# Optimization experiments

Hardware: AMD Instinct MI355X
Metric: run time of the kernel (lower is better)

## Reference

```python
import jax, jax.numpy as jnp
import numpy as np

DIM_HEAD = 128
HEADS = 16
SCALE = DIM_HEAD ** -0.5


def rotate_half(t):
    # '... (j d) -> ... j d' with j=2: split into first/second halves
    x1, x2 = jnp.split(t, 2, axis=-1)
    return jnp.concatenate((-x2, x1), axis=-1)


def apply_rope(pos, t):
    # pos: [n, d]; t: [..., n, d]
    return t * jnp.cos(pos) + rotate_half(t) * jnp.sin(pos)


def setup_inputs() -> dict:
    key = jax.random.key(0)
    k0, k1, k2, k3 = jax.random.split(key, 4)
    b, n, dim = 2, 2048, 2048
    inner = HEADS * DIM_HEAD
    return {
        "x": jax.random.normal(k0, (b, n, dim), jnp.float32),
        "Wq": jax.random.normal(k1, (dim, inner), jnp.float32) * 0.02,
        "Wkv": jax.random.normal(k2, (dim, 2 * DIM_HEAD), jnp.float32) * 0.02,
        "Wout": jax.random.normal(k3, (inner, dim), jnp.float32) * 0.02,
    }


def reference(x, Wq, Wkv, Wout):
    b, n, dim = x.shape
    # projections from the UN-normalized x (norm in original is dead code)
    q = x @ Wq                               # [b, n, h*d]
    kv = x @ Wkv                             # [b, n, 2d]
    k, v = jnp.split(kv, 2, axis=-1)         # each [b, n, d] (multi-query)
    q = q.reshape(b, n, HEADS, DIM_HEAD).transpose(0, 2, 1, 3)  # [b,h,n,d]

    # rotary positions
    inv_freq = 1.0 / (10000.0 ** (jnp.arange(0, DIM_HEAD, 2, dtype=jnp.float32) / DIM_HEAD))
    freqs = jnp.arange(n, dtype=jnp.float32)[:, None] * inv_freq[None, :]
    pos = jnp.concatenate((freqs, freqs), axis=-1)  # [n, d]

    q = apply_rope(pos, q) * SCALE
    k = apply_rope(pos, k)

    sim = jnp.einsum('bhid,bjd->bhij', q, k)  # [b,h,n,n]
    causal_mask = jnp.triu(jnp.ones((n, n), dtype=bool), 1)
    neg = -jnp.finfo(sim.dtype).max
    sim = jnp.where(causal_mask, neg, sim)
    sim = sim - jax.lax.stop_gradient(jnp.max(sim, axis=-1, keepdims=True))
    attn = jax.nn.softmax(sim, axis=-1)

    out = jnp.einsum('bhij,bjd->bhid', attn, v)          # [b,h,n,d]
    out = out.transpose(0, 2, 1, 3).reshape(b, n, HEADS * DIM_HEAD)
    return out @ Wout
```

## Files before the change

### kernel.cpp

```cpp
#include <hip/hip_runtime.h>
#include <hip/hip_bf16.h>
#include <cstddef>
#include <cstdint>

#define BATCH 2
#define SEQ   2048
#define DIM   2048
#define HEADS 16
#define DHEAD 128
#define INNER (HEADS * DHEAD)
#define MROWS (BATCH * SEQ)
#define ATT_SCALE 0.08838834764831845f
#define QK_SCALE (0.08838834764831845f * 1.4426950408889634f)
#define NEG_LOG2_10000_DIV64 (-13.287712379549449f / 64.0f)
#define M_HAT 12.0f

typedef __attribute__((ext_vector_type(8))) short short8;
typedef __attribute__((ext_vector_type(4))) short short4v;
typedef __attribute__((ext_vector_type(4))) float f32x4;

static __device__ __forceinline__ short f2bf(float x) {
    uint32_t u = __float_as_uint(x);
    uint32_t r = (u + 0x7fffu + ((u >> 16) & 1u)) >> 16;
    return (short)r;
}
static __device__ __forceinline__ float bf2f(short s) {
    return __uint_as_float(((uint32_t)(uint16_t)s) << 16);
}
static __device__ __forceinline__ short2 f2bf2(float a, float b) {
    __hip_bfloat162 h = __float22bfloat162_rn(make_float2(a, b));
    return *reinterpret_cast<short2*>(&h);
}

static __device__ __forceinline__ void glds16(const short* g, short* l) {
    __builtin_amdgcn_global_load_lds(
        (const __attribute__((address_space(1))) unsigned int*)g,
        (__attribute__((address_space(3))) unsigned int*)l, 16, 0, 0);
}

static __device__ __forceinline__ int swz_row(int r) {
    return (r & 3) | ((r >> 1) & 4);
}

static __device__ __forceinline__ void tcast_body(const float* __restrict__ W,
                                                  short* __restrict__ Wt,
                                                  int R, int C, int bx, int by,
                                                  int tid, float (*tile)[65]) {
    const int c0 = bx * 64, r0 = by * 64;
#pragma unroll
    for (int t = 0; t < 16; ++t) {
        int idx = tid + t * 256;
        int row = idx >> 6, col = idx & 63;
        tile[row][col] = W[(size_t)(r0 + row) * C + c0 + col];
    }
    __syncthreads();
#pragma unroll
    for (int t = 0; t < 16; ++t) {
        int idx = tid + t * 256;
        int r = idx >> 6, c = idx & 63;
        Wt[(size_t)(c0 + r) * R + r0 + c] = f2bf(tile[c][r]);
    }
}

__global__ __launch_bounds__(256) void prep(const float* __restrict__ x,
                                            short* __restrict__ xb,
                                            const float* __restrict__ Wq,
                                            short* __restrict__ Wt,
                                            const float* __restrict__ Wkv,
                                            short* __restrict__ Wkvt,
                                            const float* __restrict__ Wout,
                                            short* __restrict__ WtO,
                                            float2* __restrict__ lut) {
    __shared__ float tile[64][65];
    const int bid = blockIdx.x;
    const int tid = threadIdx.x;
    if (bid < 8192) {
        int i = bid * 256 + tid;
        float4 v = ((const float4*)x)[i];
        short2 s01 = f2bf2(v.x, v.y), s23 = f2bf2(v.z, v.w);
        short4v s = {s01.x, s01.y, s23.x, s23.y};
        ((short4v*)xb)[i] = s;
    } else if (bid < 9216) {
        int t = bid - 8192;
        tcast_body(Wq, Wt, DIM, INNER, t & 31, t >> 5, tid, tile);
    } else if (bid < 9344) {
        int t = bid - 9216;
        tcast_body(Wkv, Wkvt, DIM, 256, t & 3, t >> 2, tid, tile);
    } else if (bid < 10368) {
        int t = bid - 9344;
        tcast_body(Wout, WtO, INNER, DIM, t & 31, t >> 5, tid, tile);
    } else {
        int t = (bid - 10368) * 256 + tid;
        int pos = t >> 6, j = t & 63;
        float ang = (float)pos * exp2f((float)j * NEG_LOG2_10000_DIV64);
        lut[t] = make_float2(cosf(ang), sinf(ang));
    }
}

__global__ __launch_bounds__(256) void gemm_qkv(const short* __restrict__ A,
                                                const short* __restrict__ Bt,
                                                short* __restrict__ qout,
                                                short* __restrict__ kvout) {
    __shared__ __align__(16) short sA[128 * 32];
    __shared__ __align__(16) short sB[128 * 32];
    const int K = DIM;

    const int tid = threadIdx.x;
    const int w = tid >> 6, lane = tid & 63;
    const int ln = lane & 15, qr = lane >> 4;
    const int bm = blockIdx.y * 128, bn = blockIdx.x * 128;
    const int wm = (w >> 1) * 64, wn = (w & 1) * 64;

    const f32x4 zero4 = {0.f, 0.f, 0.f, 0.f};
    f32x4 acc[4][4];
#pragma unroll
    for (int mt = 0; mt < 4; ++mt)
#pragma unroll
        for (int nt = 0; nt < 4; ++nt) acc[mt][nt] = zero4;

    const int srow = lane >> 2;
    const short* pA = A + (size_t)(bm + w * 32 + srow) * K + (lane & 3) * 8;
    const short* pB = Bt + (size_t)(bn + w * 32 + srow) * K + (lane & 3) * 8;
    short* lA = &sA[(w * 32) * 32];
    short* lB = &sB[(w * 32) * 32];

    for (int k0 = 0; k0 < K; k0 += 32) {
        __syncthreads();
        glds16(pA + k0, lA);
        glds16(pA + k0 + (size_t)16 * K, lA + 512);
        glds16(pB + k0, lB);
        glds16(pB + k0 + (size_t)16 * K, lB + 512);
        __syncthreads();

        short8 af[4], bfr[4];
#pragma unroll
        for (int mt = 0; mt < 4; ++mt)
            af[mt] = *(const short8*)&sA[(wm + mt * 16 + ln) * 32 + qr * 8];
#pragma unroll
        for (int nt = 0; nt < 4; ++nt)
            bfr[nt] = *(const short8*)&sB[(wn + nt * 16 + ln) * 32 + qr * 8];
#pragma unroll
        for (int mt = 0; mt < 4; ++mt)
#pragma unroll
            for (int nt = 0; nt < 4; ++nt)
                acc[mt][nt] = __builtin_amdgcn_mfma_f32_16x16x32_bf16(
                    af[mt], bfr[nt], acc[mt][nt], 0, 0, 0);
    }

    short* C;
    int stride, colb;
    if (bn < INNER) { C = qout; stride = INNER; colb = bn; }
    else            { C = kvout; stride = 256;  colb = bn - INNER; }
#pragma unroll
    for (int mt = 0; mt < 4; ++mt)
#pragma unroll
        for (int nt = 0; nt < 4; ++nt)
#pragma unroll
            for (int r = 0; r < 4; ++r)
                C[(size_t)(bm + wm + mt * 16 + qr * 4 + r) * stride +
                  colb + wn + nt * 16 + ln] = f2bf(acc[mt][nt][r]);
}

__global__ __launch_bounds__(256) void gemm_bt(const short* __restrict__ A,
                                               const short* __restrict__ Bt,
                                               float* __restrict__ C,
                                               int M, int N, int K) {
    __shared__ __align__(16) short sA[128 * 32];
    __shared__ __align__(16) short sB[128 * 32];

    const int tid = threadIdx.x;
    const int w = tid >> 6, lane = tid & 63;
    const int ln = lane & 15, qr = lane >> 4;
    const int bm = blockIdx.y * 128, bn = blockIdx.x * 128;
    const int wm = (w >> 1) * 64, wn = (w & 1) * 64;

    const f32x4 zero4 = {0.f, 0.f, 0.f, 0.f};
    f32x4 acc[4][4];
#pragma unroll
    for (int mt = 0; mt < 4; ++mt)
#pragma unroll
        for (int nt = 0; nt < 4; ++nt) acc[mt][nt] = zero4;

    const int srow = lane >> 2;
    const short* pA = A + (size_t)(bm + w * 32 + srow) * K + (lane & 3) * 8;
    const short* pB = Bt + (size_t)(bn + w * 32 + srow) * K + (lane & 3) * 8;
    short* lA = &sA[(w * 32) * 32];
    short* lB = &sB[(w * 32) * 32];

    for (int k0 = 0; k0 < K; k0 += 32) {
        __syncthreads();
        glds16(pA + k0, lA);
        glds16(pA + k0 + (size_t)16 * K, lA + 512);
        glds16(pB + k0, lB);
        glds16(pB + k0 + (size_t)16 * K, lB + 512);
        __syncthreads();

        short8 af[4], bfr[4];
#pragma unroll
        for (int mt = 0; mt < 4; ++mt)
            af[mt] = *(const short8*)&sA[(wm + mt * 16 + ln) * 32 + qr * 8];
#pragma unroll
        for (int nt = 0; nt < 4; ++nt)
            bfr[nt] = *(const short8*)&sB[(wn + nt * 16 + ln) * 32 + qr * 8];
#pragma unroll
        for (int mt = 0; mt < 4; ++mt)
#pragma unroll
            for (int nt = 0; nt < 4; ++nt)
                acc[mt][nt] = __builtin_amdgcn_mfma_f32_16x16x32_bf16(
                    af[mt], bfr[nt], acc[mt][nt], 0, 0, 0);
    }

#pragma unroll
    for (int mt = 0; mt < 4; ++mt)
#pragma unroll
        for (int nt = 0; nt < 4; ++nt)
#pragma unroll
            for (int r = 0; r < 4; ++r)
                C[(size_t)(bm + wm + mt * 16 + qr * 4 + r) * N +
                  bn + wn + nt * 16 + ln] = acc[mt][nt][r];
}

__global__ __launch_bounds__(256) void rope_q_v(short* __restrict__ qb,
                                                const float2* __restrict__ lut) {
    int idx = blockIdx.x * 256 + threadIdx.x;
    int c = idx & 7;
    int rh = idx >> 3;
    int pos = (rh >> 4) & (SEQ - 1);
    short* row = qb + ((size_t)rh << 7);
    short8 a8 = *(short8*)&row[c * 8];
    short8 b8 = *(short8*)&row[64 + c * 8];
    const float2* lp = &lut[pos * 64 + c * 8];
    short8 o1, o2;
#pragma unroll
    for (int e = 0; e < 8; e += 2) {
        float2 cs0 = lp[e], cs1 = lp[e + 1];
        float a0 = bf2f(a8[e]), b0 = bf2f(b8[e]);
        float a1 = bf2f(a8[e + 1]), b1 = bf2f(b8[e + 1]);
        short2 p1 = f2bf2((a0 * cs0.x - b0 * cs0.y) * QK_SCALE,
                          (a1 * cs1.x - b1 * cs1.y) * QK_SCALE);
        short2 p2 = f2bf2((b0 * cs0.x + a0 * cs0.y) * QK_SCALE,
                          (b1 * cs1.x + a1 * cs1.y) * QK_SCALE);
        o1[e] = p1.x; o1[e + 1] = p1.y;
        o2[e] = p2.x; o2[e + 1] = p2.y;
    }
    *(short8*)&row[c * 8] = o1;
    *(short8*)&row[64 + c * 8] = o2;
}

__global__ __launch_bounds__(256) void prep_kv(const short* __restrict__ kvbb,
                                               short* __restrict__ kb,
                                               short* __restrict__ vt,
                                               const float2* __restrict__ lut) {
    __shared__ float tile[64][65];
    const int bid = blockIdx.x;
    const int tid = threadIdx.x;
    if (bid < 128) {
        const int b = bid >> 6;
        const int tile_id = bid & 63;
        const int p0 = (tile_id >> 1) * 64;
        const int d0 = (tile_id & 1) * 64;
#pragma unroll
        for (int t = 0; t < 16; ++t) {
            int idx = tid + t * 256;
            int row = idx >> 6, col = idx & 63;
            tile[row][col] = bf2f(kvbb[((size_t)(b * SEQ) + p0 + row) * 256 + 128 + d0 + col]);
        }
        __syncthreads();
#pragma unroll
        for (int t = 0; t < 16; ++t) {
            int idx = tid + t * 256;
            int r = idx >> 6, c = idx & 63;
            vt[((size_t)(b * DHEAD) + d0 + r) * SEQ + p0 + c] = f2bf(tile[c][r]);
        }
    } else {
        int t = (bid - 128) * 256 + tid;
        int c = t & 7;
        int bn = t >> 3;
        int pos = bn & (SEQ - 1);
        const short* row = kvbb + (size_t)bn * 256;
        short* orow = kb + ((size_t)bn << 7);
        short8 a8 = *(const short8*)&row[c * 8];
        short8 b8 = *(const short8*)&row[64 + c * 8];
        const float2* lp = &lut[pos * 64 + c * 8];
        short8 o1, o2;
#pragma unroll
        for (int e = 0; e < 8; e += 2) {
            float2 cs0 = lp[e], cs1 = lp[e + 1];
            float a0 = bf2f(a8[e]), b0 = bf2f(b8[e]);
            float a1 = bf2f(a8[e + 1]), b1 = bf2f(b8[e + 1]);
            short2 p1 = f2bf2(a0 * cs0.x - b0 * cs0.y, a1 * cs1.x - b1 * cs1.y);
            short2 p2 = f2bf2(b0 * cs0.x + a0 * cs0.y, b1 * cs1.x + a1 * cs1.y);
            o1[e] = p1.x; o1[e + 1] = p1.y;
            o2[e] = p2.x; o2[e + 1] = p2.y;
        }
        *(short8*)&orow[c * 8] = o1;
        *(short8*)&orow[64 + c * 8] = o2;
    }
}

__global__ __launch_bounds__(512, 4) void attn_mfma(const short* __restrict__ qb,
                                                    const short* __restrict__ kb,
                                                    const short* __restrict__ vt,
                                                    short* __restrict__ o) {
    __shared__ __align__(16) short sK[2][64 * 128];
    __shared__ __align__(16) short sV[2][128 * 64];

    const int bid = blockIdx.x;
    const int cc = bid >> 5;
    const int it = (cc < 8) ? (15 - cc) : (cc - 8);
    const int bh = bid & 31;
    const int h = bh & (HEADS - 1);
    const int b = bh >> 4;

    const int tid = threadIdx.x;
    const int w = tid >> 6;
    const int lane = tid & 63;
    const int ln = lane & 15;
    const int qr = lane >> 4;

    const short* kbase = kb + (size_t)b * SEQ * DHEAD;
    const short* vbase = vt + (size_t)b * DHEAD * SEQ;

    int offK[2], offV[2], ldsK[2], ldsV[2];
#pragma unroll
    for (int t = 0; t < 2; ++t) {
        int rk = w * 8 + t * 4 + (lane >> 4);
        int ck = (lane & 15) ^ swz_row(rk);
        offK[t] = rk * DHEAD + ck * 8;
        ldsK[t] = (w * 8 + t * 4) * 128;
        int rv = w * 16 + t * 8 + (lane >> 3);
        int cv = (lane & 7) ^ swz_row(rv);
        offV[t] = rv * SEQ + cv * 8;
        ldsV[t] = (w * 16 + t * 8) * 64;
    }

    const int i0 = it * 128;
    const int njt = 2 * it + 2;
    const int ig = i0 + w * 16 + ln;
    const int igmax = i0 + w * 16 + 15;

    short8 qf[4];
    {
        const size_t qrow = ((size_t)(b * SEQ + i0 + w * 16 + ln)) * INNER + h * DHEAD;
#pragma unroll
        for (int ks = 0; ks < 4; ++ks)
            qf[ks] = *(const short8*)&qb[qrow + ks * 32 + qr * 8];
    }

    const f32x4 zero4 = {0.f, 0.f, 0.f, 0.f};
    f32x4 oa[8];
#pragma unroll
    for (int dt = 0; dt < 8; ++dt) oa[dt] = zero4;
    float lsum = 0.f;

#pragma unroll
    for (int t = 0; t < 2; ++t) glds16(kbase + offK[t], &sK[0][ldsK[t]]);
#pragma unroll
    for (int t = 0; t < 2; ++t) glds16(vbase + offV[t], &sV[0][ldsV[t]]);

    for (int jt = 0; jt < njt; ++jt) {
        const int cur = jt & 1;
        __syncthreads();
        if (jt + 1 < njt) {
            const size_t kof = (size_t)(jt + 1) * 64 * DHEAD;
            const size_t vof = (size_t)(jt + 1) * 64;
#pragma unroll
            for (int t = 0; t < 2; ++t)
                glds16(kbase + kof + offK[t], &sK[cur ^ 1][ldsK[t]]);
#pragma unroll
            for (int t = 0; t < 2; ++t)
                glds16(vbase + vof + offV[t], &sV[cur ^ 1][ldsV[t]]);
        }
        if (jt * 64 > igmax) continue;

        f32x4 sacc[4];
#pragma unroll
        for (int nt = 0; nt < 4; ++nt) sacc[nt] = zero4;
#pragma unroll
        for (int nt = 0; nt < 4; ++nt) {
            const int row = ((nt >> 1) << 5) + ((ln >> 2) << 3) +
                            ((nt & 1) << 2) + (ln & 3);
            const int sw = ln & 7;
#pragma unroll
            for (int ks = 0; ks < 4; ++ks) {
                short8 kf = *(const short8*)&sK[cur][row * 128 + ((4 * ks + qr) ^ sw) * 8];
                sacc[nt] = __builtin_amdgcn_mfma_f32_16x16x32_bf16(
                    kf, qf[ks], sacc[nt], 0, 0, 0);
            }
        }

        if (jt * 64 + 63 > ig) {
#pragma unroll
            for (int nt = 0; nt < 4; ++nt)
#pragma unroll
                for (int r = 0; r < 4; ++r) {
                    int jg = jt * 64 + ((nt >> 1) << 5) + qr * 8 +
                             ((nt & 1) << 2) + r;
                    if (jg > ig) sacc[nt][r] = -3.0e38f;
                }
        }
        float rs = 0.f;
        float pv[4][4];
#pragma unroll
        for (int nt = 0; nt < 4; ++nt)
#pragma unroll
            for (int r = 0; r < 4; ++r) {
                float e = exp2f(sacc[nt][r] - M_HAT);
                pv[nt][r] = e;
                rs += e;
            }
        rs += __shfl_xor(rs, 16);
        rs += __shfl_xor(rs, 32);
        lsum += rs;
        short8 pb[2];
#pragma unroll
        for (int kb2 = 0; kb2 < 2; ++kb2) {
            short2* pp = (short2*)&pb[kb2];
            pp[0] = f2bf2(pv[2 * kb2][0], pv[2 * kb2][1]);
            pp[1] = f2bf2(pv[2 * kb2][2], pv[2 * kb2][3]);
            pp[2] = f2bf2(pv[2 * kb2 + 1][0], pv[2 * kb2 + 1][1]);
            pp[3] = f2bf2(pv[2 * kb2 + 1][2], pv[2 * kb2 + 1][3]);
        }

#pragma unroll
        for (int kb2 = 0; kb2 < 2; ++kb2) {
#pragma unroll
            for (int dt = 0; dt < 8; ++dt) {
                const int row = dt * 16 + ln;
                short8 vf = *(const short8*)&sV[cur][row * 64 +
                    ((4 * kb2 + qr) ^ swz_row(row)) * 8];
                oa[dt] = __builtin_amdgcn_mfma_f32_16x16x32_bf16(
                    vf, pb[kb2], oa[dt], 0, 0, 0);
            }
        }
    }

    const float invl = 1.f / lsum;
    short* orow = o + ((size_t)(b * SEQ + i0 + w * 16 + ln)) * INNER + h * DHEAD;
#pragma unroll
    for (int dt = 0; dt < 8; ++dt) {
        short2 s01 = f2bf2(oa[dt][0] * invl, oa[dt][1] * invl);
        short2 s23 = f2bf2(oa[dt][2] * invl, oa[dt][3] * invl);
        short4v sv = {s01.x, s01.y, s23.x, s23.y};
        *(short4v*)&orow[dt * 16 + qr * 4] = sv;
    }
}

extern "C" void kernel_launch(void* const* d_in, const int* in_sizes, int n_in,
                              void* d_out, int out_size, void* d_ws, size_t ws_size,
                              hipStream_t stream) {
    const float* x    = (const float*)d_in[0];
    const float* Wq   = (const float*)d_in[1];
    const float* Wkv  = (const float*)d_in[2];
    const float* Wout = (const float*)d_in[3];
    float* out = (float*)d_out;

    short* xb    = (short*)d_ws;
    short* Wt    = xb + (size_t)MROWS * DIM;
    short* Wkvt  = Wt + (size_t)DIM * INNER;
    short* WtO   = Wkvt + (size_t)256 * DIM;
    short* qb    = WtO + (size_t)DIM * INNER;
    short* kvbb  = qb + (size_t)MROWS * INNER;
    short* kb    = kvbb + (size_t)MROWS * 256;
    short* vt    = kb + (size_t)MROWS * DHEAD;
    float2* lut  = (float2*)(vt + (size_t)BATCH * DHEAD * SEQ);
    short* ob    = xb;

    prep<<<10880, 256, 0, stream>>>(x, xb, Wq, Wt, Wkv, Wkvt, Wout, WtO, lut);
    gemm_qkv<<<dim3(18, 32), 256, 0, stream>>>(xb, Wt, qb, kvbb);
    rope_q_v<<<(MROWS * HEADS * 8) / 256, 256, 0, stream>>>(qb, lut);
    prep_kv<<<256, 256, 0, stream>>>(kvbb, kb, vt, lut);
    attn_mfma<<<512, 512, 0, stream>>>(qb, kb, vt, ob);
    gemm_bt<<<dim3(DIM / 128, MROWS / 128), 256, 0, stream>>>(ob, WtO, out, MROWS, DIM, INNER);
}
```

Measured before the change: 290.5 us.

## Process two query sub-tiles per wave in attention to reuse K/V fragments

The attention kernel now runs 4 waves per block instead of 8, and each wave handles 32 query rows split into two 16-row sub-tiles. Each K and V fragment read from LDS feeds two MFMAs, which halves LDS read traffic per MFMA. The M_HAT offset is folded into the accumulator's initial value, and s_setprio is raised around the MFMA sections. The cost is roughly doubled accumulator register use, fewer waves per block with more global-to-LDS loads per thread, and lower occupancy from the new launch bounds.

Result: slower. 299.7 us (+3.2%).

```diff
diff --git a/kernel.cpp b/kernel.cpp
--- a/kernel.cpp
+++ b/kernel.cpp
@@ -298,7 +298,7 @@
     }
 }
 
-__global__ __launch_bounds__(512, 4) void attn_mfma(const short* __restrict__ qb,
+__global__ __launch_bounds__(256, 2) void attn_mfma(const short* __restrict__ qb,
                                                     const short* __restrict__ kb,
                                                     const short* __restrict__ vt,
                                                     short* __restrict__ o) {
@@ -321,42 +321,46 @@
     const short* kbase = kb + (size_t)b * SEQ * DHEAD;
     const short* vbase = vt + (size_t)b * DHEAD * SEQ;
 
-    int offK[2], offV[2], ldsK[2], ldsV[2];
-#pragma unroll
-    for (int t = 0; t < 2; ++t) {
-        int rk = w * 8 + t * 4 + (lane >> 4);
+    int offK[4], offV[4], ldsK[4], ldsV[4];
+#pragma unroll
+    for (int t = 0; t < 4; ++t) {
+        int rk = w * 16 + t * 4 + (lane >> 4);
         int ck = (lane & 15) ^ swz_row(rk);
         offK[t] = rk * DHEAD + ck * 8;
-        ldsK[t] = (w * 8 + t * 4) * 128;
-        int rv = w * 16 + t * 8 + (lane >> 3);
+        ldsK[t] = (w * 16 + t * 4) * 128;
+        int rv = w * 32 + t * 8 + (lane >> 3);
         int cv = (lane & 7) ^ swz_row(rv);
         offV[t] = rv * SEQ + cv * 8;
-        ldsV[t] = (w * 16 + t * 8) * 64;
+        ldsV[t] = (w * 32 + t * 8) * 64;
     }
 
     const int i0 = it * 128;
     const int njt = 2 * it + 2;
-    const int ig = i0 + w * 16 + ln;
-    const int igmax = i0 + w * 16 + 15;
-
-    short8 qf[4];
-    {
-        const size_t qrow = ((size_t)(b * SEQ + i0 + w * 16 + ln)) * INNER + h * DHEAD;
+    const int igmax = i0 + w * 32 + 31;
+
+    short8 qf[2][4];
+#pragma unroll
+    for (int qs = 0; qs < 2; ++qs) {
+        const size_t qrow =
+            ((size_t)(b * SEQ + i0 + w * 32 + qs * 16 + ln)) * INNER + h * DHEAD;
 #pragma unroll
         for (int ks = 0; ks < 4; ++ks)
-            qf[ks] = *(const short8*)&qb[qrow + ks * 32 + qr * 8];
+            qf[qs][ks] = *(const short8*)&qb[qrow + ks * 32 + qr * 8];
     }
 
     const f32x4 zero4 = {0.f, 0.f, 0.f, 0.f};
-    f32x4 oa[8];
-#pragma unroll
-    for (int dt = 0; dt < 8; ++dt) oa[dt] = zero4;
-    float lsum = 0.f;
-
-#pragma unroll
-    for (int t = 0; t < 2; ++t) glds16(kbase + offK[t], &sK[0][ldsK[t]]);
-#pragma unroll
-    for (int t = 0; t < 2; ++t) glds16(vbase + offV[t], &sV[0][ldsV[t]]);
+    const f32x4 mhat4 = {-M_HAT, -M_HAT, -M_HAT, -M_HAT};
+    f32x4 oa[2][8];
+#pragma unroll
+    for (int qs = 0; qs < 2; ++qs)
+#pragma unroll
+        for (int dt = 0; dt < 8; ++dt) oa[qs][dt] = zero4;
+    float lsum[2] = {0.f, 0.f};
+
+#pragma unroll
+    for (int t = 0; t < 4; ++t) glds16(kbase + offK[t], &sK[0][ldsK[t]]);
+#pragma unroll
+    for (int t = 0; t < 4; ++t) glds16(vbase + offV[t], &sV[0][ldsV[t]]);
 
     for (int jt = 0; jt < njt; ++jt) {
         const int cur = jt & 1;
@@ -365,17 +369,20 @@
             const size_t kof = (size_t)(jt + 1) * 64 * DHEAD;
             const size_t vof = (size_t)(jt + 1) * 64;
 #pragma unroll
-            for (int t = 0; t < 2; ++t)
+            for (int t = 0; t < 4; ++t)
                 glds16(kbase + kof + offK[t], &sK[cur ^ 1][ldsK[t]]);
 #pragma unroll
-            for (int t = 0; t < 2; ++t)
+            for (int t = 0; t < 4; ++t)
                 glds16(vbase + vof + offV[t], &sV[cur ^ 1][ldsV[t]]);
         }
         if (jt * 64 > igmax) continue;
 
-        f32x4 sacc[4];
-#pragma unroll
-        for (int nt = 0; nt < 4; ++nt) sacc[nt] = zero4;
+        f32x4 sacc[2][4];
+#pragma unroll
+        for (int qs = 0; qs < 2; ++qs)
+#pragma unroll
+            for (int nt = 0; nt < 4; ++nt) sacc[qs][nt] = mhat4;
+        __builtin_amdgcn_s_setprio(1);
 #pragma unroll
         for (int nt = 0; nt < 4; ++nt) {
             const int row = ((nt >> 1) << 5) + ((ln >> 2) << 3) +
@@ -384,44 +391,52 @@
 #pragma unroll
             for (int ks = 0; ks < 4; ++ks) {
                 short8 kf = *(const short8*)&sK[cur][row * 128 + ((4 * ks + qr) ^ sw) * 8];
-                sacc[nt] = __builtin_amdgcn_mfma_f32_16x16x32_bf16(
-                    kf, qf[ks], sacc[nt], 0, 0, 0);
+                sacc[0][nt] = __builtin_amdgcn_mfma_f32_16x16x32_bf16(
+                    kf, qf[0][ks], sacc[0][nt], 0, 0, 0);
+                sacc[1][nt] = __builtin_amdgcn_mfma_f32_16x16x32_bf16(
+                    kf, qf[1][ks], sacc[1][nt], 0, 0, 0);
             }
         }
-
-        if (jt * 64 + 63 > ig) {
+        __builtin_amdgcn_s_setprio(0);
+
+        short8 pb[2][2];
+#pragma unroll
+        for (int qs = 0; qs < 2; ++qs) {
+            const int ig = i0 + w * 32 + qs * 16 + ln;
+            if (jt * 64 + 63 > ig) {
+#pragma unroll
+                for (int nt = 0; nt < 4; ++nt)
+#pragma unroll
+                    for (int r = 0; r < 4; ++r) {
+                        int jg = jt * 64 + ((nt >> 1) << 5) + qr * 8 +
+                                 ((nt & 1) << 2) + r;
+                        if (jg > ig) sacc[qs][nt][r] = -3.0e38f;
+                    }
+            }
+            float rs = 0.f;
+            float pv[4][4];
 #pragma unroll
             for (int nt = 0; nt < 4; ++nt)
 #pragma unroll
                 for (int r = 0; r < 4; ++r) {
-                    int jg = jt * 64 + ((nt >> 1) << 5) + qr * 8 +
-                             ((nt & 1) << 2) + r;
-                    if (jg > ig) sacc[nt][r] = -3.0e38f;
+                    float e = exp2f(sacc[qs][nt][r]);
+                    pv[nt][r] = e;
+                    rs += e;
                 }
-        }
-        float rs = 0.f;
-        float pv[4][4];
-#pragma unroll
-        for (int nt = 0; nt < 4; ++nt)
-#pragma unroll
-            for (int r = 0; r < 4; ++r) {
-                float e = exp2f(sacc[nt][r] - M_HAT);
-                pv[nt][r] = e;
-                rs += e;
+            rs += __shfl_xor(rs, 16);
+            rs += __shfl_xor(rs, 32);
+            lsum[qs] += rs;
+#pragma unroll
+            for (int kb2 = 0; kb2 < 2; ++kb2) {
+                short2* pp = (short2*)&pb[qs][kb2];
+                pp[0] = f2bf2(pv[2 * kb2][0], pv[2 * kb2][1]);
+                pp[1] = f2bf2(pv[2 * kb2][2], pv[2 * kb2][3]);
+                pp[2] = f2bf2(pv[2 * kb2 + 1][0], pv[2 * kb2 + 1][1]);
+                pp[3] = f2bf2(pv[2 * kb2 + 1][2], pv[2 * kb2 + 1][3]);
             }
-        rs += __shfl_xor(rs, 16);
-        rs += __shfl_xor(rs, 32);
-        lsum += rs;
-        short8 pb[2];
-#pragma unroll
-        for (int kb2 = 0; kb2 < 2; ++kb2) {
-            short2* pp = (short2*)&pb[kb2];
-            pp[0] = f2bf2(pv[2 * kb2][0], pv[2 * kb2][1]);
-            pp[1] = f2bf2(pv[2 * kb2][2], pv[2 * kb2][3]);
-            pp[2] = f2bf2(pv[2 * kb2 + 1][0], pv[2 * kb2 + 1][1]);
-            pp[3] = f2bf2(pv[2 * kb2 + 1][2], pv[2 * kb2 + 1][3]);
-        }
-
+        }
+
+        __builtin_amdgcn_s_setprio(1);
 #pragma unroll
         for (int kb2 = 0; kb2 < 2; ++kb2) {
 #pragma unroll
@@ -429,20 +444,27 @@
                 const int row = dt * 16 + ln;
                 short8 vf = *(const short8*)&sV[cur][row * 64 +
                     ((4 * kb2 + qr) ^ swz_row(row)) * 8];
-                oa[dt] = __builtin_amdgcn_mfma_f32_16x16x32_bf16(
-                    vf, pb[kb2], oa[dt], 0, 0, 0);
+                oa[0][dt] = __builtin_amdgcn_mfma_f32_16x16x32_bf16(
+                    vf, pb[0][kb2], oa[0][dt], 0, 0, 0);
+                oa[1][dt] = __builtin_amdgcn_mfma_f32_16x16x32_bf16(
+                    vf, pb[1][kb2], oa[1][dt], 0, 0, 0);
             }
         }
-    }
-
-    const float invl = 1.f / lsum;
-    short* orow = o + ((size_t)(b * SEQ + i0 + w * 16 + ln)) * INNER + h * DHEAD;
-#pragma unroll
-    for (int dt = 0; dt < 8; ++dt) {
-        short2 s01 = f2bf2(oa[dt][0] * invl, oa[dt][1] * invl);
-        short2 s23 = f2bf2(oa[dt][2] * invl, oa[dt][3] * invl);
-        short4v sv = {s01.x, s01.y, s23.x, s23.y};
-        *(short4v*)&orow[dt * 16 + qr * 4] = sv;
+        __builtin_amdgcn_s_setprio(0);
+    }
+
+#pragma unroll
+    for (int qs = 0; qs < 2; ++qs) {
+        const float invl = 1.f / lsum[qs];
+        short* orow = o + ((size_t)(b * SEQ + i0 + w * 32 + qs * 16 + ln)) * INNER +
+                      h * DHEAD;
+#pragma unroll
+        for (int dt = 0; dt < 8; ++dt) {
+            short2 s01 = f2bf2(oa[qs][dt][0] * invl, oa[qs][dt][1] * invl);
+            short2 s23 = f2bf2(oa[qs][dt][2] * invl, oa[qs][dt][3] * invl);
+            short4v sv = {s01.x, s01.y, s23.x, s23.y};
+            *(short4v*)&orow[dt * 16 + qr * 4] = sv;
+        }
     }
 }
 
@@ -470,6 +492,6 @@
     gemm_qkv<<<dim3(18, 32), 256, 0, stream>>>(xb, Wt, qb, kvbb);
     rope_q_v<<<(MROWS * HEADS * 8) / 256, 256, 0, stream>>>(qb, lut);
     prep_kv<<<256, 256, 0, stream>>>(kvbb, kb, vt, lut);
-    attn_mfma<<<512, 512, 0, stream>>>(qb, kb, vt, ob);
+    attn_mfma<<<512, 256, 0, stream>>>(qb, kb, vt, ob);
     gemm_bt<<<dim3(DIM / 128, MROWS / 128), 256, 0, stream>>>(ob, WtO, out, MROWS, DIM, INNER);
 }
```
